# Kernel tuning notes

Measured on AMD Instinct MI355X. Metric: run time of the kernel, lower is better.

## Reference

```python
import jax, jax.numpy as jnp
import numpy as np


def setup_inputs() -> dict:
    key = jax.random.key(0)
    k1, k2, k3, k4 = jax.random.split(key, 4)
    B, N, d, E = 4, 768, 16, 12288
    emb_nodes = jax.random.normal(k1, (B, N, d), dtype=jnp.float32)
    edges = jax.random.randint(k2, (B, 2, E), 0, N, dtype=jnp.int64)
    # nn.Linear(2*d, 1): weight [1, 2d], bias [1]
    W = jax.random.normal(k3, (2 * d,), dtype=jnp.float32) * 0.1
    b = jax.random.normal(k4, (1,), dtype=jnp.float32) * 0.1
    return {"emb_nodes": emb_nodes, "edges": edges, "W": W, "b": b}


def reference(emb_nodes, edges, W, b):
    B, N, d = emb_nodes.shape
    # all-pairs (i, j): i = repeat_interleave, j = tile  -> [B, N*N, d]
    inter = jnp.repeat(emb_nodes, N, axis=1)
    rep = jnp.tile(emb_nodes, (1, N, 1))
    # original detaches the pair embeddings before the decoder
    edge_embeddings = jax.lax.stop_gradient(jnp.concatenate([inter, rep], axis=-1))  # [B, N*N, 2d]
    logits = edge_embeddings @ W + b[0]  # [B, N*N]
    # self-loop detection via embedding equality (|e_i - e_j| sum == 0)
    non_empty = jnp.abs(inter - rep).sum(axis=-1) != 0
    logits = jnp.where(non_empty, logits, jnp.float32(-10.0))
    # ground-truth edge indicator: scatter 1 at flat index i*N + j
    flat = edges[:, 0] * N + edges[:, 1]  # [B, E]
    truth = jnp.zeros((B, N * N), dtype=emb_nodes.dtype)
    truth = truth.at[jnp.arange(B)[:, None], flat].set(1.0)
    return (edge_embeddings, logits, truth)
```

## Files before the change

### kernel.cpp

```cpp
#include <hip/hip_runtime.h>

constexpr int B = 4;
constexpr int N = 768;
constexpr int D = 16;
constexpr int E = 12288;
constexpr int NN = N * N;
constexpr int PAIRS = B * NN;
constexpr long long EE_FLOATS = (long long)PAIRS * 2 * D;

__global__ void ee_fill_kernel(const float4* __restrict__ emb4,
                               float4* __restrict__ out4, int total4) {
    int idx = blockIdx.x * blockDim.x + threadIdx.x;
    if (idx >= total4) return;
    int pair = idx >> 3;
    int q = idx & 7;
    int b = pair / NN;
    int rem = pair - b * NN;
    int i = rem / N;
    int j = rem - i * N;
    int node = (q < 4) ? i : j;
    out4[idx] = emb4[((b * N + node) << 2) + (q & 3)];
}

__global__ void logits_kernel(const float4* __restrict__ emb4,
                              const float* __restrict__ W,
                              const float* __restrict__ bias,
                              float* __restrict__ logits,
                              float* __restrict__ truth, int total) {
    int p = blockIdx.x * blockDim.x + threadIdx.x;
    if (p >= total) return;
    int b = p / NN;
    int rem = p - b * NN;
    int i = rem / N;
    int j = rem - i * N;
    const float4* ei = emb4 + ((b * N + i) << 2);
    const float4* ej = emb4 + ((b * N + j) << 2);
    float acc = 0.f;
    float diff = 0.f;
#pragma unroll
    for (int q = 0; q < 4; ++q) {
        float4 a = ei[q];
        float4 c = ej[q];
        const float* w1 = W + q * 4;
        const float* w2 = W + D + q * 4;
        acc += a.x * w1[0] + a.y * w1[1] + a.z * w1[2] + a.w * w1[3];
        acc += c.x * w2[0] + c.y * w2[1] + c.z * w2[2] + c.w * w2[3];
        diff += fabsf(a.x - c.x) + fabsf(a.y - c.y) +
                fabsf(a.z - c.z) + fabsf(a.w - c.w);
    }
    acc += bias[0];
    logits[p] = (diff != 0.f) ? acc : -10.0f;
    truth[p] = 0.0f;
}

__global__ void truth_scatter_kernel(const int* __restrict__ edges,
                                     float* __restrict__ truth) {
    int t = blockIdx.x * blockDim.x + threadIdx.x;
    if (t >= B * E) return;
    int b = t / E;
    int e = t - b * E;
    int src = edges[b * 2 * E + e];
    int dst = edges[b * 2 * E + E + e];
    truth[(long long)b * NN + src * N + dst] = 1.0f;
}

extern "C" void kernel_launch(void* const* d_in, const int* in_sizes, int n_in,
                              void* d_out, int out_size, void* d_ws, size_t ws_size,
                              hipStream_t stream) {
    const float4* emb4 = (const float4*)d_in[0];
    const int* edges = (const int*)d_in[1];
    const float* W = (const float*)d_in[2];
    const float* bias = (const float*)d_in[3];

    float* out = (float*)d_out;
    float* ee = out;
    float* logits = out + EE_FLOATS;
    float* truth = out + EE_FLOATS + (long long)PAIRS;

    {
        int total4 = PAIRS * 8;
        int threads = 256;
        int blocks = (total4 + threads - 1) / threads;
        ee_fill_kernel<<<blocks, threads, 0, stream>>>(emb4, (float4*)ee, total4);
    }
    {
        int threads = 256;
        int blocks = (PAIRS + threads - 1) / threads;
        logits_kernel<<<blocks, threads, 0, stream>>>(emb4, W, bias, logits, truth, PAIRS);
    }
    {
        int threads = 256;
        int blocks = (B * E + threads - 1) / threads;
        truth_scatter_kernel<<<blocks, threads, 0, stream>>>(edges, truth);
    }
}
```

Baseline: 331.3 us.

## Fuse edge-embedding fill and logits into one per-row kernel with nontemporal stores

Replaces the separate edge-embedding fill kernel and logits kernel with a single kernel that runs one block per (batch, i) row. Each block writes the row's pair embeddings, logits and zeroed truth. It hoists the i-side embedding and its partial dot product out of the inner loop and drops the per-element div/mod index math. Stores use nontemporal hints to stream the large output past the caches. Each block covers a fixed N columns, so the kernel depends on N being a multiple of 256.

```diff
diff --git a/kernel.cpp b/kernel.cpp
--- a/kernel.cpp
+++ b/kernel.cpp
@@ -8,49 +8,68 @@
 constexpr int PAIRS = B * NN;
 constexpr long long EE_FLOATS = (long long)PAIRS * 2 * D;
 
-__global__ void ee_fill_kernel(const float4* __restrict__ emb4,
-                               float4* __restrict__ out4, int total4) {
-    int idx = blockIdx.x * blockDim.x + threadIdx.x;
-    if (idx >= total4) return;
-    int pair = idx >> 3;
-    int q = idx & 7;
-    int b = pair / NN;
-    int rem = pair - b * NN;
-    int i = rem / N;
-    int j = rem - i * N;
-    int node = (q < 4) ? i : j;
-    out4[idx] = emb4[((b * N + node) << 2) + (q & 3)];
-}
+typedef float v4f __attribute__((ext_vector_type(4)));
 
-__global__ void logits_kernel(const float4* __restrict__ emb4,
-                              const float* __restrict__ W,
-                              const float* __restrict__ bias,
-                              float* __restrict__ logits,
-                              float* __restrict__ truth, int total) {
-    int p = blockIdx.x * blockDim.x + threadIdx.x;
-    if (p >= total) return;
-    int b = p / NN;
-    int rem = p - b * NN;
-    int i = rem / N;
-    int j = rem - i * N;
-    const float4* ei = emb4 + ((b * N + i) << 2);
-    const float4* ej = emb4 + ((b * N + j) << 2);
-    float acc = 0.f;
-    float diff = 0.f;
+__global__ __launch_bounds__(256) void fused_row_kernel(
+    const v4f* __restrict__ emb4,
+    const float* __restrict__ W,
+    const float* __restrict__ bias,
+    v4f* __restrict__ ee4,
+    float* __restrict__ logits,
+    float* __restrict__ truth)
+{
+    const int blk = blockIdx.x;
+    const int b = blk / N;
+    const int i = blk - b * N;
+    const int t = threadIdx.x;
+
+    const v4f* embB = emb4 + (b * N) * 4;
+
+    const long long base = ((long long)(b * NN + i * N)) * 8;
+    const int q = t & 7;
+    v4f vi = {0.f, 0.f, 0.f, 0.f};
+    if (q < 4) vi = embB[i * 4 + q];
+    const int jq = q - 4;
 #pragma unroll
-    for (int q = 0; q < 4; ++q) {
-        float4 a = ei[q];
-        float4 c = ej[q];
-        const float* w1 = W + q * 4;
-        const float* w2 = W + D + q * 4;
-        acc += a.x * w1[0] + a.y * w1[1] + a.z * w1[2] + a.w * w1[3];
-        acc += c.x * w2[0] + c.y * w2[1] + c.z * w2[2] + c.w * w2[3];
-        diff += fabsf(a.x - c.x) + fabsf(a.y - c.y) +
-                fabsf(a.z - c.z) + fabsf(a.w - c.w);
+    for (int iter = 0; iter < (N * 8) / 256; ++iter) {
+        const int k = t + iter * 256;
+        v4f v;
+        if (q < 4) {
+            v = vi;
+        } else {
+            const int j = k >> 3;
+            v = embB[j * 4 + jq];
+        }
+        __builtin_nontemporal_store(v, &ee4[base + k]);
     }
-    acc += bias[0];
-    logits[p] = (diff != 0.f) ? acc : -10.0f;
-    truth[p] = 0.0f;
+
+    const v4f i0 = embB[i * 4 + 0], i1 = embB[i * 4 + 1],
+              i2 = embB[i * 4 + 2], i3 = embB[i * 4 + 3];
+    const float acc_i =
+        i0.x * W[0]  + i0.y * W[1]  + i0.z * W[2]  + i0.w * W[3]  +
+        i1.x * W[4]  + i1.y * W[5]  + i1.z * W[6]  + i1.w * W[7]  +
+        i2.x * W[8]  + i2.y * W[9]  + i2.z * W[10] + i2.w * W[11] +
+        i3.x * W[12] + i3.y * W[13] + i3.z * W[14] + i3.w * W[15] +
+        bias[0];
+    const long long lbase = (long long)b * NN + (long long)i * N;
+#pragma unroll
+    for (int rep = 0; rep < N / 256; ++rep) {
+        const int j = t + rep * 256;
+        const v4f j0 = embB[j * 4 + 0], j1 = embB[j * 4 + 1],
+                  j2 = embB[j * 4 + 2], j3 = embB[j * 4 + 3];
+        const float acc = acc_i +
+            j0.x * W[16] + j0.y * W[17] + j0.z * W[18] + j0.w * W[19] +
+            j1.x * W[20] + j1.y * W[21] + j1.z * W[22] + j1.w * W[23] +
+            j2.x * W[24] + j2.y * W[25] + j2.z * W[26] + j2.w * W[27] +
+            j3.x * W[28] + j3.y * W[29] + j3.z * W[30] + j3.w * W[31];
+        const float diff =
+            fabsf(i0.x - j0.x) + fabsf(i0.y - j0.y) + fabsf(i0.z - j0.z) + fabsf(i0.w - j0.w) +
+            fabsf(i1.x - j1.x) + fabsf(i1.y - j1.y) + fabsf(i1.z - j1.z) + fabsf(i1.w - j1.w) +
+            fabsf(i2.x - j2.x) + fabsf(i2.y - j2.y) + fabsf(i2.z - j2.z) + fabsf(i2.w - j2.w) +
+            fabsf(i3.x - j3.x) + fabsf(i3.y - j3.y) + fabsf(i3.z - j3.z) + fabsf(i3.w - j3.w);
+        __builtin_nontemporal_store((diff != 0.f) ? acc : -10.0f, &logits[lbase + j]);
+        __builtin_nontemporal_store(0.0f, &truth[lbase + j]);
+    }
 }
 
 __global__ void truth_scatter_kernel(const int* __restrict__ edges,
@@ -67,7 +86,7 @@
 extern "C" void kernel_launch(void* const* d_in, const int* in_sizes, int n_in,
                               void* d_out, int out_size, void* d_ws, size_t ws_size,
                               hipStream_t stream) {
-    const float4* emb4 = (const float4*)d_in[0];
+    const v4f* emb4 = (const v4f*)d_in[0];
     const int* edges = (const int*)d_in[1];
     const float* W = (const float*)d_in[2];
     const float* bias = (const float*)d_in[3];
@@ -77,17 +96,9 @@
     float* logits = out + EE_FLOATS;
     float* truth = out + EE_FLOATS + (long long)PAIRS;
 
-    {
-        int total4 = PAIRS * 8;
-        int threads = 256;
-        int blocks = (total4 + threads - 1) / threads;
-        ee_fill_kernel<<<blocks, threads, 0, stream>>>(emb4, (float4*)ee, total4);
-    }
-    {
-        int threads = 256;
-        int blocks = (PAIRS + threads - 1) / threads;
-        logits_kernel<<<blocks, threads, 0, stream>>>(emb4, W, bias, logits, truth, PAIRS);
-    }
+    fused_row_kernel<<<B * N, 256, 0, stream>>>(emb4, W, bias,
+                                                (v4f*)ee, logits, truth);
+
     {
         int threads = 256;
         int blocks = (B * E + threads - 1) / threads;
```

After: 335.9 us. About the same (+1.4%).
